# Kernel optimization log

Hardware: AMD Instinct MI355X
Metric: run time of the kernel (lower is better)

Reference implementation:

```python
import jax, jax.numpy as jnp
import numpy as np

N_NODES = 10000
N_EDGES = 160000
N_GRAPHS = 20
IN_F, HID, OUT_F, HEADS = 50, 256, 121, 4
NEG_SLOPE = 0.2
GN_EPS = 1e-5
SM_EPS = 1e-16


def _with_self_loops(edge_index, n):
    loop = jnp.arange(n, dtype=edge_index.dtype)
    src = jnp.concatenate([edge_index[0], loop])
    dst = jnp.concatenate([edge_index[1], loop])
    return src, dst


def gat_conv(x, W, att_src, att_dst, bias, src, dst, heads, out_c):
    # PyG GATConv: linear -> per-node attention halves -> edge leaky_relu
    # -> softmax over incoming edges of each dst -> weighted scatter-sum.
    n = x.shape[0]
    h = (x @ W).reshape(n, heads, out_c)                # [N,H,C]
    a_s = (h * att_src).sum(-1)                          # [N,H]
    a_d = (h * att_dst).sum(-1)                          # [N,H]
    e = a_s[src] + a_d[dst]                              # [E,H]
    e = jnp.where(e > 0, e, NEG_SLOPE * e)
    e_max = jax.ops.segment_max(e, dst, num_segments=n)  # self-loops cover all dst
    ex = jnp.exp(e - e_max[dst])
    den = jax.ops.segment_sum(ex, dst, num_segments=n)
    alpha = ex / (den[dst] + SM_EPS)                     # [E,H]
    out = jax.ops.segment_sum(h[src] * alpha[..., None], dst, num_segments=n)
    return out.reshape(n, heads * out_c) + bias


def graph_norm(x, batch, weight, bias, mean_scale, n_graphs):
    cnt = jax.ops.segment_sum(jnp.ones((x.shape[0],), x.dtype), batch,
                              num_segments=n_graphs)[:, None]    # [G,1]
    mean = jax.ops.segment_sum(x, batch, num_segments=n_graphs) / cnt
    ctr = x - mean[batch] * mean_scale
    var = jax.ops.segment_sum(ctr * ctr, batch, num_segments=n_graphs) / cnt
    inv = jax.lax.rsqrt(var + GN_EPS)
    return weight * ctr * inv[batch] + bias


def setup_inputs() -> dict:
    key = jax.random.key(0)
    ks = jax.random.split(key, 24)
    d = {}
    d['x'] = jax.random.normal(ks[0], (N_NODES, IN_F), jnp.float32)
    d['edge_index'] = jax.random.randint(ks[1], (2, N_EDGES), 0, N_NODES, jnp.int64 if jax.config.jax_enable_x64 else jnp.int32)
    d['batch'] = jnp.sort(jax.random.randint(ks[2], (N_NODES,), 0, N_GRAPHS))
    def glorot(k, shape):
        fan = shape[0] + shape[-1]
        return jax.random.normal(k, shape, jnp.float32) * np.sqrt(2.0 / fan)
    dims = [(IN_F, HEADS, HID), (HEADS * HID, HEADS, HID), (HEADS * HID, HEADS, HID), (HEADS * HID, 1, OUT_F)]
    i = 3
    for li, (fin, h, c) in enumerate(dims, 1):
        d[f'W{li}'] = glorot(ks[i], (fin, h * c)); i += 1
        d[f'as{li}'] = glorot(ks[i], (h, c)); i += 1
        d[f'ad{li}'] = glorot(ks[i], (h, c)); i += 1
        d[f'b{li}'] = jnp.zeros((h * c,), jnp.float32)
    for li in (1, 2, 3):
        w = HEADS * HID
        d[f'gw{li}'] = jnp.ones((w,), jnp.float32)
        d[f'gb{li}'] = jnp.zeros((w,), jnp.float32)
        d[f'ga{li}'] = jnp.ones((w,), jnp.float32)
    return d


def reference(x, edge_index, batch,
              W1, as1, ad1, b1, W2, as2, ad2, b2, W3, as3, ad3, b3, W4, as4, ad4, b4,
              gw1, gb1, ga1, gw2, gb2, ga2, gw3, gb3, ga3):
    src, dst = _with_self_loops(edge_index, N_NODES)
    h = gat_conv(x, W1, as1, ad1, b1, src, dst, HEADS, HID)
    h = jax.nn.elu(graph_norm(h, batch, gw1, gb1, ga1, N_GRAPHS))
    h = gat_conv(h, W2, as2, ad2, b2, src, dst, HEADS, HID)
    h = jax.nn.elu(graph_norm(h, batch, gw2, gb2, ga2, N_GRAPHS))
    h = gat_conv(h, W3, as3, ad3, b3, src, dst, HEADS, HID)
    h = jax.nn.elu(graph_norm(h, batch, gw3, gb3, ga3, N_GRAPHS))
    return gat_conv(h, W4, as4, ad4, b4, src, dst, 1, OUT_F)
```

## Files before the change

kernel.cpp:

```cpp
#include <hip/hip_runtime.h>
#include <math.h>

#define NN 10000
#define NE 160000
#define E2 (NE + NN)
#define NG 20
#define MPAD 10112
#define NSPLIT 8

typedef __attribute__((ext_vector_type(8))) short short8;
typedef __attribute__((ext_vector_type(4))) float f32x4;

__device__ inline unsigned short f2bf(float f){
  unsigned u = __float_as_uint(f);
  unsigned r = u + 0x7FFFu + ((u >> 16) & 1u);
  return (unsigned short)(r >> 16);
}
__device__ inline float bf2f(unsigned short h){ return __uint_as_float(((unsigned)h) << 16); }

__device__ inline void gload_lds16(const void* g, void* l){
  __builtin_amdgcn_global_load_lds((const __attribute__((address_space(1))) void*)g,
                                   (__attribute__((address_space(3))) void*)l, 16, 0, 0);
}

__global__ void k_gptr(const int* __restrict__ batch, int* __restrict__ gptr){
  int g = threadIdx.x;
  if (g > NG) return;
  int lo = 0, hi = NN;
  while (lo < hi){ int mid = (lo+hi)>>1; if (batch[mid] < g) lo = mid+1; else hi = mid; }
  gptr[g] = lo;
}

__global__ void k_count(const int* __restrict__ ei, int* __restrict__ cnt){
  int e = blockIdx.x*256 + threadIdx.x;
  if (e >= E2) return;
  int d = (e < NE) ? ei[NE + e] : (e - NE);
  atomicAdd(&cnt[d], 1);
}

__global__ void k_scan(const int* __restrict__ cnt, int* __restrict__ ptr){
  __shared__ int tpre[256];
  __shared__ int tsum[256];
  int tid = threadIdx.x;
  const int per = (NN + 255)/256;
  int base = tid*per;
  int s = 0;
  for (int i=0;i<per;i++){ int idx=base+i; if (idx<NN) s += cnt[idx]; }
  tsum[tid] = s;
  __syncthreads();
  if (tid == 0){
    int run = 0;
    for (int i=0;i<256;i++){ tpre[i]=run; run += tsum[i]; }
    ptr[NN] = run;
  }
  __syncthreads();
  int run = tpre[tid];
  for (int i=0;i<per;i++){ int idx=base+i; if (idx<NN){ ptr[idx]=run; run += cnt[idx]; } }
}

__global__ void k_copy(const int* __restrict__ src, int* __restrict__ dst){
  int i = blockIdx.x*256 + threadIdx.x;
  if (i < NN) dst[i] = src[i];
}

__global__ void k_scatter(const int* __restrict__ ei, int* __restrict__ fill, int* __restrict__ csrc){
  int e = blockIdx.x*256 + threadIdx.x;
  if (e >= E2) return;
  int s, d;
  if (e < NE){ s = ei[e]; d = ei[NE + e]; } else { s = d = e - NE; }
  int pos = atomicAdd(&fill[d], 1);
  csrc[pos] = s;
}

__global__ void k_xconv(const float* __restrict__ x, unsigned short* __restrict__ xbf){
  int i = blockIdx.x*256 + threadIdx.x;
  if (i >= MPAD*64) return;
  int r = i >> 6, c = i & 63;
  float v = (r < NN && c < 50) ? x[r*50 + c] : 0.f;
  xbf[i] = f2bf(v);
}

#define WT0 0
#define WT1 65536
#define WT2 1114112
#define WT3 2162688
#define WTT 2293760
__global__ void k_wconvall(const float* __restrict__ W0, const float* __restrict__ W1,
                           const float* __restrict__ W2, const float* __restrict__ W3,
                           unsigned short* __restrict__ wt){
  int i = blockIdx.x*256 + threadIdx.x;
  if (i >= WTT) return;
  const float* W; int K, N, Kpad, off;
  if (i < WT1){ W=W0; K=50; N=1024; Kpad=64; off=WT0; }
  else if (i < WT2){ W=W1; K=1024; N=1024; Kpad=1024; off=WT1; }
  else if (i < WT3){ W=W2; K=1024; N=1024; Kpad=1024; off=WT2; }
  else { W=W3; K=1024; N=121; Kpad=1024; off=WT3; }
  int j = i - off;
  int nn = j / Kpad, kk = j - nn*Kpad;
  float v = (nn < N && kk < K) ? W[(size_t)kk*N + nn] : 0.f;
  wt[i] = f2bf(v);
}

template<int TBM, int TBN>
__global__ __launch_bounds__(256) void k_mfma_gemm(
    const unsigned short* __restrict__ A,
    const unsigned short* __restrict__ Bt,
    unsigned short* __restrict__ Cbf,
    int M, int K, int FS, int ncb)
{
  constexpr int MFR = TBM/32;
  constexpr int NFR = TBN/32;
  constexpr int ABYTES = TBM*64;
  constexpr int BBYTES = TBN*64;
  constexpr int LPS = TBM/64 + TBN/64;
  __shared__ unsigned short sA[3*TBM*32];
  __shared__ unsigned short sB[3*TBN*32];
  const int tid = threadIdx.x;
  const int wave = tid >> 6;
  const int lane = tid & 63;
  const int nwg = gridDim.x;
  const int q = nwg >> 3, rmod = nwg & 7;
  const int xcd = blockIdx.x & 7, idx = blockIdx.x >> 3;
  const int wg = (xcd < rmod) ? (xcd*(q+1) + idx) : (rmod*(q+1) + (xcd - rmod)*q + idx);
  const int rowt = wg / ncb;
  const int colt = wg - rowt*ncb;
  const int row0 = rowt * TBM;
  const int col0 = colt * TBN;
  const int wr = (wave >> 1) * (TBM/2);
  const int wc = (wave & 1) * (TBN/2);
  f32x4 acc[MFR][NFR];
  #pragma unroll
  for (int i=0;i<MFR;i++)
    #pragma unroll
    for (int j=0;j<NFR;j++){ acc[i][j][0]=0.f; acc[i][j][1]=0.f; acc[i][j][2]=0.f; acc[i][j][3]=0.f; }

  const int arow = tid >> 2;
  const int achn = (tid & 3) ^ ((arow >> 1) & 3);
  const unsigned short* aSrc = A + (size_t)(row0 + arow)*K + achn*8;
  const unsigned short* bSrc = Bt + (size_t)(col0 + arow)*K + achn*8;
  char* ldsA = (char*)sA + wave*1024;
  char* ldsB = (char*)sB + wave*1024;

  auto STAGE = [&](int k0, int buf){
    #pragma unroll
    for (int h=0; h<TBM/64; h++) gload_lds16(aSrc + (size_t)h*64*K + k0, ldsA + buf*ABYTES + h*4096);
    #pragma unroll
    for (int h=0; h<TBN/64; h++) gload_lds16(bSrc + (size_t)h*64*K + k0, ldsB + buf*BBYTES + h*4096);
  };

  const int NT = K >> 5;
  const int kch = lane >> 4;
  const int rlo = lane & 15;

  STAGE(0, 0);
  STAGE(32, 1);

  int cur = 0;
  for (int t = 0; t < NT; ++t){
    asm volatile("s_waitcnt lgkmcnt(0)" ::: "memory");
    if (t+1 < NT){
      if constexpr (LPS==4)      asm volatile("s_waitcnt vmcnt(4)" ::: "memory");
      else if constexpr (LPS==3) asm volatile("s_waitcnt vmcnt(3)" ::: "memory");
      else                       asm volatile("s_waitcnt vmcnt(2)" ::: "memory");
    } else {
      asm volatile("s_waitcnt vmcnt(0)" ::: "memory");
    }
    __builtin_amdgcn_sched_barrier(0);
    __builtin_amdgcn_s_barrier();
    __builtin_amdgcn_sched_barrier(0);
    const unsigned short* bA = sA + cur*(TBM*32);
    const unsigned short* bB = sB + cur*(TBN*32);
    short8 af[MFR], bfr[NFR];
    #pragma unroll
    for (int m=0;m<MFR;m++){
      int r = wr + m*16 + rlo;
      af[m] = *(const short8*)(bA + r*32 + ((kch ^ ((r>>1)&3))<<3));
    }
    #pragma unroll
    for (int n=0;n<NFR;n++){
      int r = wc + n*16 + rlo;
      bfr[n] = *(const short8*)(bB + r*32 + ((kch ^ ((r>>1)&3))<<3));
    }
    if (t+2 < NT){
      int nb = cur + 2; if (nb >= 3) nb -= 3;
      STAGE((t+2) << 5, nb);
    }
    __builtin_amdgcn_s_setprio(1);
    #pragma unroll
    for (int m=0;m<MFR;m++)
      #pragma unroll
      for (int n=0;n<NFR;n++)
        acc[m][n] = __builtin_amdgcn_mfma_f32_16x16x32_bf16(af[m], bfr[n], acc[m][n], 0, 0, 0);
    __builtin_amdgcn_s_setprio(0);
    cur += 1; if (cur == 3) cur = 0;
  }
  const int cr = (lane >> 4) * 4;
  const int cc = lane & 15;
  #pragma unroll
  for (int m=0;m<MFR;m++){
    #pragma unroll
    for (int n=0;n<NFR;n++){
      int col = col0 + wc + n*16 + cc;
      #pragma unroll
      for (int r=0;r<4;r++){
        int row = row0 + wr + m*16 + cr + r;
        if (row < M) Cbf[(size_t)row*FS + col] = f2bf(acc[m][n][r]);
      }
    }
  }
}

__global__ __launch_bounds__(256) void k_attprepw(
    const unsigned short* __restrict__ h,
    const float* __restrict__ atts, const float* __restrict__ attd,
    float* __restrict__ a_s, float* __restrict__ a_d)
{
  const int wid = threadIdx.x >> 6, lane = threadIdx.x & 63;
  const int node = blockIdx.x*4 + wid;
  const unsigned short* hp = h + (size_t)node*1024 + lane*16;
  short8 v0 = *(const short8*)hp;
  short8 v1 = *(const short8*)(hp+8);
  const float* sp = atts + lane*16;
  const float* dp = attd + lane*16;
  float ss = 0.f, sd = 0.f;
  #pragma unroll
  for (int j=0;j<8;j++){ float f = bf2f((unsigned short)v0[j]); ss += f*sp[j];   sd += f*dp[j]; }
  #pragma unroll
  for (int j=0;j<8;j++){ float f = bf2f((unsigned short)v1[j]); ss += f*sp[8+j]; sd += f*dp[8+j]; }
  #pragma unroll
  for (int o=8;o;o>>=1){ ss += __shfl_xor(ss,o); sd += __shfl_xor(sd,o); }
  if ((lane & 15) == 0){
    int hh = lane >> 4;
    a_s[node*4 + hh] = ss;
    a_d[node*4 + hh] = sd;
  }
}

__global__ __launch_bounds__(256) void k_attprep4(
    const unsigned short* __restrict__ h,
    const float* __restrict__ atts, const float* __restrict__ attd,
    float* __restrict__ a_s, float* __restrict__ a_d)
{
  const int wid = threadIdx.x >> 6, lane = threadIdx.x & 63;
  const int node = blockIdx.x*4 + wid;
  const unsigned short* hp = h + (size_t)node*128;
  float ss = 0.f, sd = 0.f;
  {
    float f = bf2f(hp[lane]);
    if (lane < 121){ ss += f*atts[lane]; sd += f*attd[lane]; }
  }
  int c2 = lane + 64;
  if (c2 < 121){
    float f = bf2f(hp[c2]);
    ss += f*atts[c2]; sd += f*attd[c2];
  }
  #pragma unroll
  for (int o=32;o;o>>=1){ ss += __shfl_xor(ss,o); sd += __shfl_xor(sd,o); }
  if (lane == 0){ a_s[node] = ss; a_d[node] = sd; }
}

__global__ __launch_bounds__(256) void k_gatherw(
    const unsigned short* __restrict__ h,
    const float* __restrict__ a_s, const float* __restrict__ a_d,
    const int* __restrict__ ptr, const int* __restrict__ csrc,
    const float* __restrict__ bias, float* __restrict__ out)
{
  __shared__ float sal[4][64*4];
  __shared__ int ssn[4][64];
  const int wid = threadIdx.x >> 6, lane = threadIdx.x & 63;
  const int node = blockIdx.x*4 + wid;
  const int hh = lane >> 4;
  const int beg = ptr[node], deg = ptr[node+1] - beg;
  f32x4 ad4 = *(const f32x4*)(a_d + node*4);
  float acc[16], acc2[16];
  #pragma unroll
  for (int j=0;j<16;j++){ acc[j]=0.f; acc2[j]=0.f; }
  f32x4 denp = {0.f,0.f,0.f,0.f};
  const unsigned short* hb = h + lane*16;

  for (int c0 = 0; c0 < deg; c0 += 64){
    int n = min(64, deg - c0);
    if (lane < n){
      int s = csrc[beg + c0 + lane];
      f32x4 as4 = *(const f32x4*)(a_s + s*4);
      f32x4 e4;
      #pragma unroll
      for (int k2=0;k2<4;k2++){
        float ev = as4[k2] + ad4[k2];
        ev = ev > 0.f ? ev : 0.2f*ev;
        float x = __expf(ev);
        e4[k2] = x;
        denp[k2] += x;
      }
      *(f32x4*)&sal[wid][lane*4] = e4;
      ssn[wid][lane] = s;
    }
    int e = 0;
    for (; e + 1 < n; e += 2){
      int sA_ = ssn[wid][e], sB_ = ssn[wid][e+1];
      float aA = sal[wid][e*4 + hh], aB = sal[wid][(e+1)*4 + hh];
      const unsigned short* pA = hb + (size_t)sA_*1024;
      const unsigned short* pB = hb + (size_t)sB_*1024;
      short8 uA0 = *(const short8*)pA, uA1 = *(const short8*)(pA+8);
      short8 uB0 = *(const short8*)pB, uB1 = *(const short8*)(pB+8);
      #pragma unroll
      for (int j=0;j<8;j++){ acc[j]   += bf2f((unsigned short)uA0[j])*aA;
                             acc[8+j] += bf2f((unsigned short)uA1[j])*aA; }
      #pragma unroll
      for (int j=0;j<8;j++){ acc2[j]   += bf2f((unsigned short)uB0[j])*aB;
                             acc2[8+j] += bf2f((unsigned short)uB1[j])*aB; }
    }
    if (e < n){
      int sA_ = ssn[wid][e];
      float aA = sal[wid][e*4 + hh];
      const unsigned short* pA = hb + (size_t)sA_*1024;
      short8 uA0 = *(const short8*)pA, uA1 = *(const short8*)(pA+8);
      #pragma unroll
      for (int j=0;j<8;j++){ acc[j]   += bf2f((unsigned short)uA0[j])*aA;
                             acc[8+j] += bf2f((unsigned short)uA1[j])*aA; }
    }
  }
  #pragma unroll
  for (int o=32;o;o>>=1){
    #pragma unroll
    for (int k2=0;k2<4;k2++) denp[k2] += __shfl_xor(denp[k2], o);
  }
  float inv = 1.f / (denp[hh] + 1e-16f);
  float* op = out + (size_t)node*1024 + lane*16;
  const float* bp = bias + lane*16;
  #pragma unroll
  for (int j=0;j<16;j++) op[j] = (acc[j]+acc2[j])*inv + bp[j];
}

__global__ __launch_bounds__(256) void k_gatherw1(
    const unsigned short* __restrict__ h,
    const float* __restrict__ a_s, const float* __restrict__ a_d,
    const int* __restrict__ ptr, const int* __restrict__ csrc,
    const float* __restrict__ bias, float* __restrict__ out)
{
  __shared__ float sal[4][64];
  __shared__ int ssn[4][64];
  const int wid = threadIdx.x >> 6, lane = threadIdx.x & 63;
  const int node = blockIdx.x*4 + wid;
  const int beg = ptr[node], deg = ptr[node+1] - beg;
  float ad = a_d[node];
  float den = 0.f;
  float acc[2] = {0.f,0.f}, acc2[2] = {0.f,0.f};
  const int c0i = lane*2;
  const unsigned short* hb = h + c0i;

  for (int b0 = 0; b0 < deg; b0 += 64){
    int n = min(64, deg - b0);
    if (lane < n){
      int s = csrc[beg + b0 + lane];
      float ev = a_s[s] + ad;
      ev = ev > 0.f ? ev : 0.2f*ev;
      float x = __expf(ev);
      sal[wid][lane] = x;
      ssn[wid][lane] = s;
      den += x;
    }
    int e = 0;
    for (; e + 1 < n; e += 2){
      int sA_ = ssn[wid][e], sB_ = ssn[wid][e+1];
      float aA = sal[wid][e], aB = sal[wid][e+1];
      const unsigned short* pA = hb + (size_t)sA_*128;
      const unsigned short* pB = hb + (size_t)sB_*128;
      acc[0]  += bf2f(pA[0])*aA; acc[1]  += bf2f(pA[1])*aA;
      acc2[0] += bf2f(pB[0])*aB; acc2[1] += bf2f(pB[1])*aB;
    }
    if (e < n){
      int sA_ = ssn[wid][e];
      float aA = sal[wid][e];
      const unsigned short* pA = hb + (size_t)sA_*128;
      acc[0] += bf2f(pA[0])*aA; acc[1] += bf2f(pA[1])*aA;
    }
  }
  #pragma unroll
  for (int o=32;o;o>>=1) den += __shfl_xor(den, o);
  float inv = 1.f / (den + 1e-16f);
  if (c0i < 121)   out[(size_t)node*121 + c0i]   = (acc[0]+acc2[0])*inv + bias[c0i];
  if (c0i+1 < 121) out[(size_t)node*121 + c0i+1] = (acc[1]+acc2[1])*inv + bias[c0i+1];
}

__global__ void k_gnstats(const float* __restrict__ x, const int* __restrict__ gptr,
                          float* __restrict__ psum, float* __restrict__ psq){
  int g = blockIdx.x, cc = blockIdx.y, sp = blockIdx.z;
  int c = cc*256 + threadIdx.x;
  int beg = gptr[g], end = gptr[g+1];
  int n = end - beg;
  int per = (n + NSPLIT - 1) / NSPLIT;
  int nb = beg + sp*per, ne = min(end, nb + per);
  float s = 0.f, qv = 0.f;
  for (int i = nb; i < ne; i++){ float v = x[(size_t)i*1024 + c]; s += v; qv += v*v; }
  int idx = (sp*NG + g)*1024 + c;
  psum[idx] = s; psq[idx] = qv;
}

__global__ void k_coef(const float* __restrict__ psum, const float* __restrict__ psq,
                       const int* __restrict__ gptr,
                       const float* __restrict__ w, const float* __restrict__ b, const float* __restrict__ ms,
                       float* __restrict__ cA, float* __restrict__ cB){
  int i = blockIdx.x*256 + threadIdx.x;
  if (i >= NG*1024) return;
  int g = i >> 10, c = i & 1023;
  float cntf = (float)(gptr[g+1] - gptr[g]);
  float sm = 0.f, sq = 0.f;
  #pragma unroll
  for (int sp=0; sp<NSPLIT; sp++){
    sm += psum[(sp*NG + g)*1024 + c];
    sq += psq[(sp*NG + g)*1024 + c];
  }
  float m = sm / cntf;
  float s = ms[c];
  float ex2 = sq / cntf;
  float var = ex2 - 2.f*s*m*m + s*s*m*m;
  float inv = rsqrtf(var + 1e-5f);
  float wa = w[c]*inv;
  cA[i] = wa;
  cB[i] = b[c] - wa*m*s;
}

__global__ void k_applyelu(const float* __restrict__ x, const int* __restrict__ batch,
                           const float* __restrict__ cA, const float* __restrict__ cB,
                           unsigned short* __restrict__ obf){
  size_t i = (size_t)blockIdx.x*256 + threadIdx.x;
  if (i >= (size_t)NN*1024) return;
  int node = (int)(i >> 10);
  int c = (int)(i & 1023);
  int g = batch[node];
  float y = cA[g*1024 + c]*x[i] + cB[g*1024 + c];
  y = y > 0.f ? y : expm1f(y);
  obf[i] = f2bf(y);
}

extern "C" void kernel_launch(void* const* d_in, const int* in_sizes, int n_in,
                              void* d_out, int out_size, void* d_ws, size_t ws_size,
                              hipStream_t stream){
  (void)in_sizes; (void)n_in; (void)out_size; (void)ws_size;
  const float* x     = (const float*)d_in[0];
  const int*   ei    = (const int*)d_in[1];
  const int*   batch = (const int*)d_in[2];
  const float* W[4]  = {(const float*)d_in[3],  (const float*)d_in[7],  (const float*)d_in[11], (const float*)d_in[15]};
  const float* AS[4] = {(const float*)d_in[4],  (const float*)d_in[8],  (const float*)d_in[12], (const float*)d_in[16]};
  const float* AD[4] = {(const float*)d_in[5],  (const float*)d_in[9],  (const float*)d_in[13], (const float*)d_in[17]};
  const float* BI[4] = {(const float*)d_in[6],  (const float*)d_in[10], (const float*)d_in[14], (const float*)d_in[18]};
  const float* GW[3] = {(const float*)d_in[19], (const float*)d_in[22], (const float*)d_in[25]};
  const float* GB[3] = {(const float*)d_in[20], (const float*)d_in[23], (const float*)d_in[26]};
  const float* GA[3] = {(const float*)d_in[21], (const float*)d_in[24], (const float*)d_in[27]};

  float* ws   = (float*)d_ws;
  float* bufB = ws;
  float* a_s  = bufB + (size_t)NN*1024;
  float* a_d  = a_s + (size_t)NN*4;
  float* psum = a_d + (size_t)NN*4;
  float* psq  = psum + (size_t)NSPLIT*NG*1024;
  float* cA   = psq  + (size_t)NSPLIT*NG*1024;
  float* cB   = cA   + (size_t)NG*1024;
  int* ptr  = (int*)(cB + (size_t)NG*1024);
  int* fill = ptr + (NN + 8);
  int* csrc = fill + (NN + 8);
  int* gptr = csrc + E2;
  unsigned short* abf = (unsigned short*)(gptr + 24);
  unsigned short* xbf = abf;
  unsigned short* hbf = abf + (size_t)MPAD*1024;
  unsigned short* wt  = hbf + (size_t)NN*1024;

  hipMemsetAsync(fill, 0, sizeof(int)*(NN+1), stream);
  k_gptr<<<1, 32, 0, stream>>>(batch, gptr);
  k_count<<<(E2+255)/256, 256, 0, stream>>>(ei, fill);
  k_scan<<<1, 256, 0, stream>>>(fill, ptr);
  k_copy<<<(NN+255)/256, 256, 0, stream>>>(ptr, fill);
  k_scatter<<<(E2+255)/256, 256, 0, stream>>>(ei, fill, csrc);
  k_xconv<<<(MPAD*64+255)/256, 256, 0, stream>>>(x, xbf);
  k_wconvall<<<(WTT+255)/256, 256, 0, stream>>>(W[0], W[1], W[2], W[3], wt);

  const int Kp[4]  = {64, 1024, 1024, 1024};
  const int Np[4]  = {1024, 1024, 1024, 128};
  const int Woff[4] = {WT0, WT1, WT2, WT3};
  for (int li = 0; li < 4; ++li){
    int FS = Np[li];
    const unsigned short* Ain = (li == 0) ? xbf : abf;
    const unsigned short* Wt = wt + Woff[li];
    if (li < 3){
      int ncb = Np[li]/128;
      int nwg = (MPAD/64) * ncb;
      k_mfma_gemm<64,128><<<nwg, 256, 0, stream>>>(Ain, Wt, hbf, NN, Kp[li], FS, ncb);
      k_attprepw<<<NN/4, 256, 0, stream>>>(hbf, AS[li], AD[li], a_s, a_d);
      k_gatherw<<<NN/4, 256, 0, stream>>>(hbf, a_s, a_d, ptr, csrc, BI[li], bufB);
      k_gnstats<<<dim3(NG, 4, NSPLIT), 256, 0, stream>>>(bufB, gptr, psum, psq);
      k_coef<<<(NG*1024 + 255)/256, 256, 0, stream>>>(psum, psq, gptr, GW[li], GB[li], GA[li], cA, cB);
      k_applyelu<<<(NN*1024 + 255)/256, 256, 0, stream>>>(bufB, batch, cA, cB, abf);
    } else {
      int ncb = Np[li]/64;
      int nwg = (MPAD/64) * ncb;
      k_mfma_gemm<64,64><<<nwg, 256, 0, stream>>>(Ain, Wt, hbf, NN, Kp[li], FS, ncb);
      k_attprep4<<<NN/4, 256, 0, stream>>>(hbf, AS[li], AD[li], a_s, a_d);
      k_gatherw1<<<NN/4, 256, 0, stream>>>(hbf, a_s, a_d, ptr, csrc, BI[li], (float*)d_out);
    }
  }
}
```

Baseline: 516.2 us.

## Replace GEMM with 256-row tile, 8-wave kernel for larger output tiles

Introduces a 512-thread GEMM kernel with 256x256 (or 256x128 for the last layer) block tiles, with each wave computing a 128-row slice, and pads M to 10240. It aims to raise data reuse per LDS tile and reduce global traffic for the weight and activation operands. In exchange the grid shrinks to a few dozen to 160 workgroups, which can leave many compute units idle and raises register pressure.

Result: faster. 502.9 us (-2.6%).

```diff
diff --git a/kernel.cpp b/kernel.cpp
--- a/kernel.cpp
+++ b/kernel.cpp
@@ -5,7 +5,7 @@
 #define NE 160000
 #define E2 (NE + NN)
 #define NG 20
-#define MPAD 10112
+#define MPAD 10240
 #define NSPLIT 8
 
 typedef __attribute__((ext_vector_type(8))) short short8;
@@ -101,19 +101,21 @@
   wt[i] = f2bf(v);
 }
 
-template<int TBM, int TBN>
-__global__ __launch_bounds__(256) void k_mfma_gemm(
+template<int TBN>
+__global__ __launch_bounds__(512, 2) void k_gemm256(
     const unsigned short* __restrict__ A,
     const unsigned short* __restrict__ Bt,
     unsigned short* __restrict__ Cbf,
     int M, int K, int FS, int ncb)
 {
-  constexpr int MFR = TBM/32;
-  constexpr int NFR = TBN/32;
-  constexpr int ABYTES = TBM*64;
+  constexpr int MFR = 8;
+  constexpr int NFR = TBN/64;
+  constexpr int ABYTES = 256*64;
   constexpr int BBYTES = TBN*64;
-  constexpr int LPS = TBM/64 + TBN/64;
-  __shared__ unsigned short sA[3*TBM*32];
+  constexpr int AINST = 2;
+  constexpr int BINST = TBN/128;
+  constexpr int LPS = AINST + BINST;
+  __shared__ unsigned short sA[3*256*32];
   __shared__ unsigned short sB[3*TBN*32];
   const int tid = threadIdx.x;
   const int wave = tid >> 6;
@@ -124,28 +126,42 @@
   const int wg = (xcd < rmod) ? (xcd*(q+1) + idx) : (rmod*(q+1) + (xcd - rmod)*q + idx);
   const int rowt = wg / ncb;
   const int colt = wg - rowt*ncb;
-  const int row0 = rowt * TBM;
+  const int row0 = rowt * 256;
   const int col0 = colt * TBN;
-  const int wr = (wave >> 1) * (TBM/2);
-  const int wc = (wave & 1) * (TBN/2);
+  const int wr = (wave >> 2) * 128;
+  const int wc = (wave & 3) * (TBN/4);
   f32x4 acc[MFR][NFR];
   #pragma unroll
   for (int i=0;i<MFR;i++)
     #pragma unroll
     for (int j=0;j<NFR;j++){ acc[i][j][0]=0.f; acc[i][j][1]=0.f; acc[i][j][2]=0.f; acc[i][j][3]=0.f; }
 
-  const int arow = tid >> 2;
-  const int achn = (tid & 3) ^ ((arow >> 1) & 3);
-  const unsigned short* aSrc = A + (size_t)(row0 + arow)*K + achn*8;
-  const unsigned short* bSrc = Bt + (size_t)(col0 + arow)*K + achn*8;
-  char* ldsA = (char*)sA + wave*1024;
-  char* ldsB = (char*)sB + wave*1024;
+  const unsigned short* aP[AINST];
+  int aL[AINST];
+  #pragma unroll
+  for (int i=0;i<AINST;i++){
+    int s = (wave*AINST + i)*64 + lane;
+    int row = s >> 2, chn = (s & 3) ^ ((row >> 1) & 3);
+    aP[i] = A + (size_t)(row0 + row)*K + chn*8;
+    aL[i] = (wave*AINST + i)*1024;
+  }
+  const unsigned short* bP[BINST];
+  int bL[BINST];
+  #pragma unroll
+  for (int i=0;i<BINST;i++){
+    int s = (wave*BINST + i)*64 + lane;
+    int row = s >> 2, chn = (s & 3) ^ ((row >> 1) & 3);
+    bP[i] = Bt + (size_t)(col0 + row)*K + chn*8;
+    bL[i] = (wave*BINST + i)*1024;
+  }
+  char* ldsA = (char*)sA;
+  char* ldsB = (char*)sB;
 
   auto STAGE = [&](int k0, int buf){
     #pragma unroll
-    for (int h=0; h<TBM/64; h++) gload_lds16(aSrc + (size_t)h*64*K + k0, ldsA + buf*ABYTES + h*4096);
-    #pragma unroll
-    for (int h=0; h<TBN/64; h++) gload_lds16(bSrc + (size_t)h*64*K + k0, ldsB + buf*BBYTES + h*4096);
+    for (int i=0;i<AINST;i++) gload_lds16(aP[i] + k0, ldsA + buf*ABYTES + aL[i]);
+    #pragma unroll
+    for (int i=0;i<BINST;i++) gload_lds16(bP[i] + k0, ldsB + buf*BBYTES + bL[i]);
   };
 
   const int NT = K >> 5;
@@ -159,16 +175,15 @@
   for (int t = 0; t < NT; ++t){
     asm volatile("s_waitcnt lgkmcnt(0)" ::: "memory");
     if (t+1 < NT){
-      if constexpr (LPS==4)      asm volatile("s_waitcnt vmcnt(4)" ::: "memory");
-      else if constexpr (LPS==3) asm volatile("s_waitcnt vmcnt(3)" ::: "memory");
-      else                       asm volatile("s_waitcnt vmcnt(2)" ::: "memory");
+      if constexpr (LPS==4) asm volatile("s_waitcnt vmcnt(4)" ::: "memory");
+      else                  asm volatile("s_waitcnt vmcnt(3)" ::: "memory");
     } else {
       asm volatile("s_waitcnt vmcnt(0)" ::: "memory");
     }
     __builtin_amdgcn_sched_barrier(0);
     __builtin_amdgcn_s_barrier();
     __builtin_amdgcn_sched_barrier(0);
-    const unsigned short* bA = sA + cur*(TBM*32);
+    const unsigned short* bA = sA + cur*(256*32);
     const unsigned short* bB = sB + cur*(TBN*32);
     short8 af[MFR], bfr[NFR];
     #pragma unroll
@@ -483,18 +498,18 @@
     const unsigned short* Ain = (li == 0) ? xbf : abf;
     const unsigned short* Wt = wt + Woff[li];
     if (li < 3){
-      int ncb = Np[li]/128;
-      int nwg = (MPAD/64) * ncb;
-      k_mfma_gemm<64,128><<<nwg, 256, 0, stream>>>(Ain, Wt, hbf, NN, Kp[li], FS, ncb);
+      int ncb = 1024/256;
+      int nwg = (MPAD/256) * ncb;
+      k_gemm256<256><<<nwg, 512, 0, stream>>>(Ain, Wt, hbf, NN, Kp[li], FS, ncb);
       k_attprepw<<<NN/4, 256, 0, stream>>>(hbf, AS[li], AD[li], a_s, a_d);
       k_gatherw<<<NN/4, 256, 0, stream>>>(hbf, a_s, a_d, ptr, csrc, BI[li], bufB);
       k_gnstats<<<dim3(NG, 4, NSPLIT), 256, 0, stream>>>(bufB, gptr, psum, psq);
       k_coef<<<(NG*1024 + 255)/256, 256, 0, stream>>>(psum, psq, gptr, GW[li], GB[li], GA[li], cA, cB);
       k_applyelu<<<(NN*1024 + 255)/256, 256, 0, stream>>>(bufB, batch, cA, cB, abf);
     } else {
-      int ncb = Np[li]/64;
-      int nwg = (MPAD/64) * ncb;
-      k_mfma_gemm<64,64><<<nwg, 256, 0, stream>>>(Ain, Wt, hbf, NN, Kp[li], FS, ncb);
+      int ncb = 1;
+      int nwg = (MPAD/256) * ncb;
+      k_gemm256<128><<<nwg, 512, 0, stream>>>(Ain, Wt, hbf, NN, Kp[li], FS, ncb);
       k_attprep4<<<NN/4, 256, 0, stream>>>(hbf, AS[li], AD[li], a_s, a_d);
       k_gatherw1<<<NN/4, 256, 0, stream>>>(hbf, a_s, a_d, ptr, csrc, BI[li], (float*)d_out);
     }
```
